# Optimization experiments

Measured on AMD Instinct MI355X. Metric: run time of the kernel, lower is better.

## Reference

```python
import jax, jax.numpy as jnp
import numpy as np

N, C, X, Y, Z = 2, 32, 48, 48, 24
ROI = 3  # odd, explicit center voxel
LOG_SCALE_INIT = float(np.log(1.0 / 0.07))


def _offsets():
    c = (ROI - 1) // 2
    i, j, k = jnp.meshgrid(jnp.arange(ROI), jnp.arange(ROI), jnp.arange(ROI), indexing='ij')
    return jnp.stack([i - c, j - c, k - c], axis=-1).reshape(-1, 3).astype(jnp.float32)  # (K,3)


def setup_inputs() -> dict:
    key = jax.random.key(0)
    k0, k1 = jax.random.split(key)
    gx, gy, gz = jnp.meshgrid(jnp.arange(X), jnp.arange(Y), jnp.arange(Z), indexing='ij')
    spatial_locations = jnp.stack([gx, gy, gz], axis=-1).reshape(-1, 3).astype(jnp.float32)  # (M,3)
    return {
        'voxel_feat_0': jax.random.normal(k0, (N, C, X, Y, Z), dtype=jnp.float32),
        'voxel_feat_1': jax.random.normal(k1, (N, C, X, Y, Z), dtype=jnp.float32),
        'spatial_locations': spatial_locations,
        'logit_scale': jnp.asarray(LOG_SCALE_INIT, dtype=jnp.float32),
        'training': 1,
    }


def reference(voxel_feat_0, voxel_feat_1, spatial_locations, logit_scale, training):
    n, c, xd, yd, zd = voxel_feat_0.shape
    eps = jnp.float32(1e-7)
    f0 = voxel_feat_0 / (jnp.linalg.norm(voxel_feat_0, axis=1, keepdims=True) + eps)
    f1 = voxel_feat_1 / (jnp.linalg.norm(voxel_feat_1, axis=1, keepdims=True) + eps)

    offsets = _offsets()  # (K,3)
    samp = spatial_locations[:, None, :] + offsets[None, :, :]  # (M,K,3) float coords

    # grid_sample(mode='nearest', align_corners=True, padding_mode='zeros')
    # normalize to [-1,1] then unnormalize -> round-trips to the integer coord;
    # equivalent to direct nearest-integer indexing with zeros outside the volume.
    size = jnp.array([xd, yd, zd], dtype=samp.dtype)
    unnorm = ((2.0 * samp / (size - 1.0) - 1.0) + 1.0) * 0.5 * (size - 1.0)
    idx = jnp.round(unnorm).astype(jnp.int32)  # (M,K,3)
    hi = jnp.array([xd, yd, zd], dtype=jnp.int32)
    valid = jnp.all((idx >= 0) & (idx < hi), axis=-1)  # (M,K)
    ic = jnp.clip(idx, 0, hi - 1)

    # gather sparse neighborhood features: (N,C,M,K)
    sample = f1[:, :, ic[..., 0], ic[..., 1], ic[..., 2]]
    sample = sample * valid[None, None, :, :].astype(sample.dtype)

    f0_flat = f0.reshape(n, c, -1)  # (N,C,M)
    logits = jnp.exp(logit_scale) * jnp.einsum('ncm,ncmk->nmk', f0_flat, sample)
    prob = jax.nn.softmax(logits, axis=-1)  # (N,M,K)

    if training:
        flow = jnp.einsum('nmk,kd->nmd', prob, offsets)  # soft expected offset
    else:
        flow = offsets[jnp.argmax(prob, axis=-1)]  # (N,M,3) hard argmax offset

    # src_mask is None: topk over all-ones mask selects every voxel, so the
    # gather/scatter pair is an identity permutation of the flattened grid.
    return flow.reshape(n, xd, yd, zd, 3)
```

## Files before the change

kernel.cpp:

```cpp
#include <hip/hip_runtime.h>
#include <math.h>

#define N_ 2
#define C_ 32
#define X_ 48
#define Y_ 48
#define Z_ 24
#define M_ (X_*Y_*Z_)
#define NM_ (N_*M_)

#define TX_ 2
#define TY_ 4
#define HX_ (TX_+2)
#define HY_ (TY_+2)
#define HVOX_ (HX_*HY_*Z_)
#define TVOX_ (TX_*TY_*Z_)
#define THREADS_ 384
#define NXT_ (X_/TX_)
#define NYT_ (Y_/TY_)

typedef _Float16 h2 __attribute__((ext_vector_type(2)));

#if __has_builtin(__builtin_amdgcn_fdot2)
__device__ __forceinline__ float dot2(h2 a, h2 b, float c) {
    return __builtin_amdgcn_fdot2(a, b, c, false);
}
#else
__device__ __forceinline__ float dot2(h2 a, h2 b, float c) {
    return fmaf((float)a[1], (float)b[1], fmaf((float)a[0], (float)b[0], c));
}
#endif

__global__ __launch_bounds__(THREADS_, 3) void fused_kernel(
    const float* __restrict__ f0, const float* __restrict__ f1,
    const float* __restrict__ logit_scale, float* __restrict__ out)
{
    __shared__ int4 lds[HVOX_ * 4];

    const int tid = threadIdx.x;
    const int bid = blockIdx.x;
    const int n   = bid / (NXT_ * NYT_);
    const int rem = bid - n * (NXT_ * NYT_);
    const int xt  = rem % NXT_;
    const int yt  = rem / NXT_;
    const int x0  = xt * TX_;
    const int y0  = yt * TY_;

    const float* f1b = f1 + (size_t)n * C_ * M_;
    for (int h = tid; h < HVOX_; h += THREADS_) {
        int hx = h / (HY_ * Z_);
        int rh = h - hx * (HY_ * Z_);
        int hy = rh / Z_;
        int hz = rh - hy * Z_;
        int gx = min(max(x0 - 1 + hx, 0), X_ - 1);
        int gy = min(max(y0 - 1 + hy, 0), Y_ - 1);
        int gm = (gx * Y_ + gy) * Z_ + hz;

        float b[C_];
        float s = 0.f;
#pragma unroll
        for (int c = 0; c < C_; ++c) {
            b[c] = f1b[(size_t)c * M_ + gm];
            s = fmaf(b[c], b[c], s);
        }
        float rs = 1.0f / (sqrtf(s) + 1e-7f);
#pragma unroll
        for (int q = 0; q < 4; ++q) {
            union { int4 qq; h2 hh[4]; } u;
#pragma unroll
            for (int e = 0; e < 4; ++e) {
                h2 v2;
                v2[0] = (_Float16)(b[8 * q + 2 * e]     * rs);
                v2[1] = (_Float16)(b[8 * q + 2 * e + 1] * rs);
                u.hh[e] = v2;
            }
            lds[h * 4 + (q ^ ((h >> 1) & 3))] = u.qq;
        }
    }
    __syncthreads();

    const int lane = tid & 63;
    const int w    = tid >> 6;
    const int hi   = lane >> 5;
    const int slot = lane & 31;
    const int ov   = w * 32 + slot;
    const int tz   = ov % Z_;
    const int txy  = ov / Z_;
    const int ty   = txy % TY_;
    const int tx   = txy / TY_;
    const int gx = x0 + tx, gy = y0 + ty, gz = tz;
    const int gm = (gx * Y_ + gy) * Z_ + gz;

    const float* p0 = f0 + (size_t)n * C_ * M_ + (size_t)hi * 16 * M_ + gm;
    float a[16];
    float s0 = 0.f;
#pragma unroll
    for (int i = 0; i < 16; ++i) {
        a[i] = p0[(size_t)i * M_];
        s0 = fmaf(a[i], a[i], s0);
    }
    s0 += __shfl_xor(s0, 32, 64);
    float rs0 = __expf(logit_scale[0]) / (sqrtf(s0) + 1e-7f);
    h2 A[8];
#pragma unroll
    for (int i = 0; i < 8; ++i) {
        h2 v;
        v[0] = (_Float16)(a[2 * i]     * rs0);
        v[1] = (_Float16)(a[2 * i + 1] * rs0);
        A[i] = v;
    }

    float S = 0.f, FX = 0.f, FY = 0.f, FZ = 0.f;
#pragma unroll
    for (int i = 0; i < 3; ++i)
#pragma unroll
    for (int j = 0; j < 3; ++j)
#pragma unroll
    for (int k = 0; k < 3; ++k) {
        bool val = (gx + i - 1 >= 0) & (gx + i - 1 < X_) &
                   (gy + j - 1 >= 0) & (gy + j - 1 < Y_) &
                   (gz + k - 1 >= 0) & (gz + k - 1 < Z_);
        int hz = min(max(tz + k - 1, 0), Z_ - 1);
        int v  = (tx + i) * (HY_ * Z_) + (ty + j) * Z_ + hz;
        union { int4 qq; h2 hh[4]; } B0, B1;
        int vx = (v >> 1) & 3;
        B0.qq = lds[v * 4 + ((2 * hi)     ^ vx)];
        B1.qq = lds[v * 4 + ((2 * hi + 1) ^ vx)];
        float d = 0.f;
#pragma unroll
        for (int e = 0; e < 4; ++e) d = dot2(A[e],     B0.hh[e], d);
#pragma unroll
        for (int e = 0; e < 4; ++e) d = dot2(A[4 + e], B1.hh[e], d);
        d += __shfl_xor(d, 32, 64);
        d = val ? d : 0.0f;
        float e_ = __expf(d);
        S += e_;
        if (i == 0) FX -= e_; else if (i == 2) FX += e_;
        if (j == 0) FY -= e_; else if (j == 2) FY += e_;
        if (k == 0) FZ -= e_; else if (k == 2) FZ += e_;
    }

    if (hi == 0) {
        float inv = 1.0f / S;
        size_t ob = ((size_t)n * M_ + gm) * 3;
        out[ob + 0] = FX * inv;
        out[ob + 1] = FY * inv;
        out[ob + 2] = FZ * inv;
    }
}

extern "C" void kernel_launch(void* const* d_in, const int* in_sizes, int n_in,
                              void* d_out, int out_size, void* d_ws, size_t ws_size,
                              hipStream_t stream) {
    const float* f0 = (const float*)d_in[0];
    const float* f1 = (const float*)d_in[1];
    const float* ls = (const float*)d_in[3];
    float* out = (float*)d_out;

    const int blocks = NXT_ * NYT_ * N_;
    fused_kernel<<<blocks, THREADS_, 0, stream>>>(f0, f1, ls, out);
}
```

Before: 18.25 us.

## Split z into two tiles and spread halo normalization across four threads per voxel

Tiles the volume along z as well, using a 2x4x12 tile with a z halo. This halves block size to 192 threads, doubles the block count and raises the occupancy hint to 6. The halo-load phase now gives each voxel to four threads, each loading 8 channels, with shuffles to reduce the norm, instead of one thread loading all 32 channels. The aim is more parallelism and latency hiding, in exchange for extra halo traffic from the z halo.

```diff
diff --git a/kernel.cpp b/kernel.cpp
--- a/kernel.cpp
+++ b/kernel.cpp
@@ -7,17 +7,20 @@
 #define Y_ 48
 #define Z_ 24
 #define M_ (X_*Y_*Z_)
-#define NM_ (N_*M_)
 
 #define TX_ 2
 #define TY_ 4
+#define TZ_ 12
 #define HX_ (TX_+2)
 #define HY_ (TY_+2)
-#define HVOX_ (HX_*HY_*Z_)
-#define TVOX_ (TX_*TY_*Z_)
-#define THREADS_ 384
+#define HZ_ (TZ_+2)
+#define HVOX_ (HX_*HY_*HZ_)
+#define TVOX_ (TX_*TY_*TZ_)
+#define THREADS_ 192
 #define NXT_ (X_/TX_)
 #define NYT_ (Y_/TY_)
+#define NZT_ (Z_/TZ_)
+#define P1_ITERS_ ((HVOX_*4)/THREADS_)
 
 typedef _Float16 h2 __attribute__((ext_vector_type(2)));
 
@@ -31,7 +34,7 @@
 }
 #endif
 
-__global__ __launch_bounds__(THREADS_, 3) void fused_kernel(
+__global__ __launch_bounds__(THREADS_, 6) void fused_kernel(
     const float* __restrict__ f0, const float* __restrict__ f1,
     const float* __restrict__ logit_scale, float* __restrict__ out)
 {
@@ -39,43 +42,51 @@
 
     const int tid = threadIdx.x;
     const int bid = blockIdx.x;
-    const int n   = bid / (NXT_ * NYT_);
-    const int rem = bid - n * (NXT_ * NYT_);
-    const int xt  = rem % NXT_;
-    const int yt  = rem / NXT_;
-    const int x0  = xt * TX_;
-    const int y0  = yt * TY_;
+    const int n   = bid / (NXT_ * NYT_ * NZT_);
+    int rem = bid - n * (NXT_ * NYT_ * NZT_);
+    const int zt = rem % NZT_;  rem /= NZT_;
+    const int xt = rem % NXT_;
+    const int yt = rem / NXT_;
+    const int x0 = xt * TX_;
+    const int y0 = yt * TY_;
+    const int z0 = zt * TZ_;
 
     const float* f1b = f1 + (size_t)n * C_ * M_;
-    for (int h = tid; h < HVOX_; h += THREADS_) {
-        int hx = h / (HY_ * Z_);
-        int rh = h - hx * (HY_ * Z_);
-        int hy = rh / Z_;
-        int hz = rh - hy * Z_;
-        int gx = min(max(x0 - 1 + hx, 0), X_ - 1);
-        int gy = min(max(y0 - 1 + hy, 0), Y_ - 1);
-        int gm = (gx * Y_ + gy) * Z_ + hz;
+#pragma unroll 2
+    for (int it = 0; it < P1_ITERS_; ++it) {
+        int tt = it * THREADS_ + tid;
+        int h = tt >> 2;
+        int q = tt & 3;
+        int hx = h / (HY_ * HZ_);
+        int rh = h - hx * (HY_ * HZ_);
+        int hy = rh / HZ_;
+        int hz = rh - hy * HZ_;
+        int ggx = min(max(x0 - 1 + hx, 0), X_ - 1);
+        int ggy = min(max(y0 - 1 + hy, 0), Y_ - 1);
+        int ggz = min(max(z0 - 1 + hz, 0), Z_ - 1);
+        int ggm = (ggx * Y_ + ggy) * Z_ + ggz;
 
-        float b[C_];
+        const float* p = f1b + (size_t)q * 8 * M_ + ggm;
+        float b[8];
         float s = 0.f;
 #pragma unroll
-        for (int c = 0; c < C_; ++c) {
-            b[c] = f1b[(size_t)c * M_ + gm];
-            s = fmaf(b[c], b[c], s);
+        for (int i = 0; i < 8; ++i) {
+            b[i] = p[(size_t)i * M_];
+            s = fmaf(b[i], b[i], s);
         }
+        s += __shfl_xor(s, 1, 64);
+        s += __shfl_xor(s, 2, 64);
         float rs = 1.0f / (sqrtf(s) + 1e-7f);
+
+        union { int4 qq; h2 hh[4]; } u;
 #pragma unroll
-        for (int q = 0; q < 4; ++q) {
-            union { int4 qq; h2 hh[4]; } u;
-#pragma unroll
-            for (int e = 0; e < 4; ++e) {
-                h2 v2;
-                v2[0] = (_Float16)(b[8 * q + 2 * e]     * rs);
-                v2[1] = (_Float16)(b[8 * q + 2 * e + 1] * rs);
-                u.hh[e] = v2;
-            }
-            lds[h * 4 + (q ^ ((h >> 1) & 3))] = u.qq;
+        for (int e = 0; e < 4; ++e) {
+            h2 v2;
+            v2[0] = (_Float16)(b[2 * e]     * rs);
+            v2[1] = (_Float16)(b[2 * e + 1] * rs);
+            u.hh[e] = v2;
         }
+        lds[h * 4 + (q ^ ((h >> 1) & 3))] = u.qq;
     }
     __syncthreads();
 
@@ -84,11 +95,11 @@
     const int hi   = lane >> 5;
     const int slot = lane & 31;
     const int ov   = w * 32 + slot;
-    const int tz   = ov % Z_;
-    const int txy  = ov / Z_;
+    const int tz   = ov % TZ_;
+    const int txy  = ov / TZ_;
     const int ty   = txy % TY_;
     const int tx   = txy / TY_;
-    const int gx = x0 + tx, gy = y0 + ty, gz = tz;
+    const int gx = x0 + tx, gy = y0 + ty, gz = z0 + tz;
     const int gm = (gx * Y_ + gy) * Z_ + gz;
 
     const float* p0 = f0 + (size_t)n * C_ * M_ + (size_t)hi * 16 * M_ + gm;
@@ -120,8 +131,7 @@
         bool val = (gx + i - 1 >= 0) & (gx + i - 1 < X_) &
                    (gy + j - 1 >= 0) & (gy + j - 1 < Y_) &
                    (gz + k - 1 >= 0) & (gz + k - 1 < Z_);
-        int hz = min(max(tz + k - 1, 0), Z_ - 1);
-        int v  = (tx + i) * (HY_ * Z_) + (ty + j) * Z_ + hz;
+        int v = ((tx + i) * HY_ + (ty + j)) * HZ_ + (tz + k);
         union { int4 qq; h2 hh[4]; } B0, B1;
         int vx = (v >> 1) & 3;
         B0.qq = lds[v * 4 + ((2 * hi)     ^ vx)];
@@ -157,6 +167,6 @@
     const float* ls = (const float*)d_in[3];
     float* out = (float*)d_out;
 
-    const int blocks = NXT_ * NYT_ * N_;
+    const int blocks = NXT_ * NYT_ * NZT_ * N_;
     fused_kernel<<<blocks, THREADS_, 0, stream>>>(f0, f1, ls, out);
 }
```

Measured after the change: 23.73 us. 1.3x slower.
